# Kernel optimization log

Measured on AMD Instinct MI355X. Metric: run time of the kernel, lower is better.

The kernel has to match this reference:

```python
import jax, jax.numpy as jnp
import numpy as np

DIM = 2048            # model dim
HID = 4096            # ssm inner dim (multiple_of*round(2/3*6144))
H = 64                # n_heads
P = HID // H          # head_dim = 64
N = 128               # state_dim
G = 1                 # n_groups
K = 4                 # conv_size
Q = 128               # chunk_size
CONV_DIM = HID + 2 * G * N       # 4352
D_IN = 2 * HID + 2 * G * N + H   # 8512
EPS = 1e-5


def _causal_conv_silu(xBC, w):
    # xBC: [B,L,C], w: [C,K]; depthwise causal conv1d fused with SiLU
    kern = w.T[:, None, :]  # [K,1,C]
    y = jax.lax.conv_general_dilated(
        xBC, kern, window_strides=(1,), padding=[(K - 1, 0)],
        dimension_numbers=('NHC', 'HIO', 'NHC'),
        feature_group_count=xBC.shape[-1])
    return y * jax.nn.sigmoid(y)


def _ssm(x, W_in, conv_w, dt_bias, A_log, D, norm_w, W_out):
    Bsz, L, _ = x.shape
    zxbcdt = x @ W_in.T                       # [B,L,D_IN]
    z = zxbcdt[..., :HID]                     # gate
    xBC = zxbcdt[..., HID:HID + CONV_DIM]
    dt_raw = zxbcdt[..., HID + CONV_DIM:]     # [B,L,H]

    xBC = _causal_conv_silu(xBC, conv_w)
    xs = xBC[..., :HID].reshape(Bsz, L, H, P)
    rep = H // G
    Bh = jnp.repeat(xBC[..., HID:HID + G * N].reshape(Bsz, L, G, N), rep, axis=2)  # [B,L,H,N]
    Ch = jnp.repeat(xBC[..., HID + G * N:].reshape(Bsz, L, G, N), rep, axis=2)

    dt = jax.nn.softplus(dt_raw + dt_bias)    # [B,L,H], dt_softplus=True
    A = -jnp.exp(A_log)                       # [H]

    # ---- chunked selective scan (Mamba2 SSD), chunk size Q ----
    nc = L // Q
    a = (dt * A).reshape(Bsz, nc, Q, H)
    cum = jnp.cumsum(a, axis=2)               # inclusive within-chunk cumsum, <= 0
    xs_c = xs.reshape(Bsz, nc, Q, H, P)
    dtc = dt.reshape(Bsz, nc, Q, H)
    Bc = Bh.reshape(Bsz, nc, Q, H, N)
    Cc = Ch.reshape(Bsz, nc, Q, H, N)

    # intra-chunk (diagonal) part: Y[i] += sum_{j<=i} exp(cum_i-cum_j) dt_j (C_i.B_j) x_j
    diff = cum[:, :, :, None, :] - cum[:, :, None, :, :]     # [b,c,i,j,h]
    tril = jnp.tril(jnp.ones((Q, Q), bool))[None, None, :, :, None]
    Lmat = jnp.exp(jnp.where(tril, diff, -jnp.inf))          # causal decay matrix
    CB = jnp.einsum('bcihn,bcjhn->bcijh', Cc, Bc)
    M = CB * Lmat * dtc[:, :, None, :, :]
    Yd = jnp.einsum('bcijh,bcjhp->bcihp', M, xs_c)

    # per-chunk end state: sum_j exp(cum_last-cum_j) dt_j x_j (x) B_j
    wdec = jnp.exp(cum[:, :, -1:, :] - cum) * dtc            # [b,c,q,h]
    states = jnp.einsum('bcqh,bcqhn,bcqhp->bchpn', wdec, Bc, xs_c)
    chunk_decay = jnp.exp(cum[:, :, -1, :])                  # [b,c,h]

    # inter-chunk recurrence over nc chunks
    def step(S, inp):
        dec, st = inp                                        # [b,h], [b,h,p,n]
        return S * dec[..., None, None] + st, S              # emit state entering chunk
    S0 = jnp.zeros((Bsz, H, P, N), x.dtype)
    _, Sprev = jax.lax.scan(step, S0,
                            (chunk_decay.transpose(1, 0, 2),
                             states.transpose(1, 0, 2, 3, 4)))
    Sprev = Sprev.transpose(1, 0, 2, 3, 4)                   # [b,c,h,p,n]

    # inter-chunk (off-diagonal) contribution
    Yoff = jnp.einsum('bcqh,bcqhn,bchpn->bcqhp', jnp.exp(cum), Cc, Sprev)

    y = (Yd + Yoff).reshape(Bsz, L, H, P) + D[None, None, :, None] * xs  # skip D
    y = y.reshape(Bsz, L, HID)

    yz = y * (z * jax.nn.sigmoid(z))                         # gated: y * silu(z)
    yn = yz * jax.lax.rsqrt(jnp.mean(yz * yz, axis=-1, keepdims=True) + EPS) * norm_w
    return yn @ W_out.T


def setup_inputs() -> dict:
    key = jax.random.key(0)
    k = jax.random.split(key, 6)
    return {
        'x': jax.random.normal(k[0], (2, 4096, DIM), jnp.float32),
        'W_in': jax.random.normal(k[1], (D_IN, DIM), jnp.float32) * DIM ** -0.5,
        'conv_w': jax.random.normal(k[2], (CONV_DIM, K), jnp.float32) * K ** -0.5,
        'dt_bias': jax.random.uniform(k[3], (H,), jnp.float32, minval=0.001, maxval=0.1),
        'A_log': jnp.log(jax.random.uniform(k[4], (H,), jnp.float32, minval=1.0, maxval=16.0)),
        'D': jnp.ones((H,), jnp.float32),
        'norm_w': jnp.ones((HID,), jnp.float32),
        'W_out': jax.random.normal(k[5], (DIM, HID), jnp.float32) * HID ** -0.5,
    }


def reference(x, W_in, conv_w, dt_bias, A_log, D, norm_w, W_out):
    return _ssm(x, W_in, conv_w, dt_bias, A_log, D, norm_w, W_out)
```

## Files before the change

### kernel.cpp

```cpp
#include <hip/hip_runtime.h>
#include <hip/hip_fp16.h>
#include <math.h>

#define ROWS   8192
#define DIMK   2048
#define HIDN   4096
#define QCH    128
#define NCHUNK 32

typedef __attribute__((ext_vector_type(8))) short short8;
typedef __attribute__((ext_vector_type(8))) _Float16 half8;
typedef __attribute__((ext_vector_type(4))) float floatx4;

static __device__ inline unsigned short f2h(float f){
  union { _Float16 h; unsigned short u; } v; v.h = (_Float16)f; return v.u;
}
static __device__ inline float h2f(unsigned short u){
  union { unsigned short u; _Float16 h; } v; v.u = u; return (float)v.h;
}
static __device__ inline void async_cp16(const void* g, void* l){
  __builtin_amdgcn_global_load_lds((const __attribute__((address_space(1))) void*)g,
                                   (__attribute__((address_space(3))) void*)l, 16, 0, 0);
}

__global__ void k_cast(const float* __restrict__ in, unsigned short* __restrict__ out, int n4){
  int i = blockIdx.x * 256 + threadIdx.x;
  if (i < n4){
    float4 v = ((const float4*)in)[i];
    unsigned long long p = (unsigned long long)f2h(v.x)
                         | ((unsigned long long)f2h(v.y) << 16)
                         | ((unsigned long long)f2h(v.z) << 32)
                         | ((unsigned long long)f2h(v.w) << 48);
    ((unsigned long long*)out)[i] = p;
  }
}

#define DT_KT 128
__global__ __launch_bounds__(256)
void k_dtraw(const float* __restrict__ x, const float* __restrict__ Win,
             float* __restrict__ dtraw){
  __shared__ float ws[64 * (DT_KT + 4)];
  const int t = threadIdx.x;
  const int lane = t & 63, w = t >> 6;
  const int r0 = blockIdx.x * 8;
  const int rw = __builtin_amdgcn_readfirstlane(r0 + w * 2);
  float acc0 = 0.f, acc1 = 0.f;
  for (int k0 = 0; k0 < DIMK; k0 += DT_KT){
    __syncthreads();
#pragma unroll
    for (int l = 0; l < 8; l++){
      int fidx = (l * 256 + t) * 4;
      int row = fidx >> 7, col = fidx & 127;
      *(float4*)&ws[row * 132 + col] =
          *(const float4*)&Win[(size_t)(8448 + row) * DIMK + k0 + col];
    }
    __syncthreads();
    const float* xa = x + (size_t)rw * DIMK + k0;
    const float* xb = xa + DIMK;
#pragma unroll 8
    for (int kk = 0; kk < DT_KT; kk += 4){
      float4 wv = *(const float4*)&ws[lane * 132 + kk];
      float4 va = *(const float4*)&xa[kk];
      float4 vb = *(const float4*)&xb[kk];
      acc0 += wv.x*va.x + wv.y*va.y + wv.z*va.z + wv.w*va.w;
      acc1 += wv.x*vb.x + wv.y*vb.y + wv.z*vb.z + wv.w*vb.w;
    }
  }
  dtraw[(size_t)rw * 64 + lane]       = acc0;
  dtraw[(size_t)(rw + 1) * 64 + lane] = acc1;
}

__device__ inline void gemm_core(const unsigned short* __restrict__ A,
                                 const unsigned short* __restrict__ B,
                                 int Kd, int row0, int col0,
                                 unsigned short* lA, unsigned short* lB,
                                 floatx4 (&acc)[4][4], int t){
  const int w = t >> 6, lane = t & 63;
  const int quad = lane >> 4, l16 = lane & 15;
  const int wr = (w >> 1) * 64, wc = (w & 1) * 64;
  for (int k0 = 0; k0 < Kd; k0 += 64){
#pragma unroll
    for (int i = 0; i < 4; i++){
      int cb = i * 256 + w * 64, c = cb + lane;
      async_cp16(A + (size_t)(row0 + (c >> 3)) * Kd + k0 + (c & 7) * 8, lA + (size_t)cb * 8);
    }
#pragma unroll
    for (int i = 0; i < 4; i++){
      int cb = i * 256 + w * 64, c = cb + lane;
      async_cp16(B + (size_t)(col0 + (c >> 3)) * Kd + k0 + (c & 7) * 8, lB + (size_t)cb * 8);
    }
    __syncthreads();
#pragma unroll
    for (int ks = 0; ks < 2; ks++){
      half8 af[4], bfr[4];
#pragma unroll
      for (int i = 0; i < 4; i++){
        af[i]  = *(const half8*)&lA[(wr + i*16 + l16)*64 + ks*32 + quad*8];
        bfr[i] = *(const half8*)&lB[(wc + i*16 + l16)*64 + ks*32 + quad*8];
      }
#pragma unroll
      for (int i = 0; i < 4; i++)
#pragma unroll
        for (int j = 0; j < 4; j++)
          acc[i][j] = __builtin_amdgcn_mfma_f32_16x16x32_f16(af[i], bfr[j], acc[i][j], 0, 0, 0);
    }
    __syncthreads();
  }
}

__global__ __launch_bounds__(256, 2)
void k_gemm1(const unsigned short* __restrict__ A, const unsigned short* __restrict__ B,
             unsigned short* __restrict__ zbuf, unsigned short* __restrict__ xsraw,
             unsigned short* __restrict__ bcraw){
  __shared__ __align__(16) unsigned short lA[128*64];
  __shared__ __align__(16) unsigned short lB[128*64];
  const int t = threadIdx.x;
  const int row0 = blockIdx.y * 128, col0 = blockIdx.x * 128;
  floatx4 acc[4][4] = {};
  gemm_core(A, B, DIMK, row0, col0, lA, lB, acc, t);
  const int w = t >> 6, lane = t & 63, quad = lane >> 4, l16 = lane & 15;
  const int wr = (w >> 1) * 64, wc = (w & 1) * 64;
  unsigned short* dst; int cbase, ldd;
  if (col0 < 4096){ dst = zbuf; cbase = 0; ldd = 4096; }
  else if (col0 < 8192){ dst = xsraw; cbase = 4096; ldd = 4096; }
  else { dst = bcraw; cbase = 8192; ldd = 256; }
#pragma unroll
  for (int i = 0; i < 4; i++)
#pragma unroll
    for (int j = 0; j < 4; j++){
      int rb = row0 + wr + i*16 + quad*4;
      int cc = col0 + wc + j*16 + l16 - cbase;
#pragma unroll
      for (int r = 0; r < 4; r++)
        dst[(size_t)(rb + r) * ldd + cc] = f2h(acc[i][j][r]);
    }
}

__global__ __launch_bounds__(256, 2)
void k_gemm2(const unsigned short* __restrict__ A, const unsigned short* __restrict__ B,
             float* __restrict__ C){
  __shared__ __align__(16) unsigned short lA[128*64];
  __shared__ __align__(16) unsigned short lB[128*64];
  const int t = threadIdx.x;
  const int row0 = blockIdx.y * 128, col0 = blockIdx.x * 128;
  floatx4 acc[4][4] = {};
  gemm_core(A, B, HIDN, row0, col0, lA, lB, acc, t);
  const int w = t >> 6, lane = t & 63, quad = lane >> 4, l16 = lane & 15;
  const int wr = (w >> 1) * 64, wc = (w & 1) * 64;
#pragma unroll
  for (int i = 0; i < 4; i++)
#pragma unroll
    for (int j = 0; j < 4; j++){
      int rb = row0 + wr + i*16 + quad*4;
      int cc = col0 + wc + j*16 + l16;
#pragma unroll
      for (int r = 0; r < 4; r++)
        C[(size_t)(rb + r) * DIMK + cc] = acc[i][j][r];
    }
}

__global__ void k_halo(const unsigned short* __restrict__ xsraw, unsigned short* __restrict__ halo){
  int col = blockIdx.x * 256 + threadIdx.x;
  int slot = blockIdx.y, bc = blockIdx.z;
  long r = (long)bc * QCH - 3 + slot;
  if (r >= 0)
    halo[((size_t)bc * 3 + slot) * 4096 + col] = xsraw[(size_t)r * 4096 + col];
}

__global__ void k_convbc(const unsigned short* __restrict__ bcraw, const float* __restrict__ cw,
                         unsigned short* __restrict__ bcc){
  int row = blockIdx.x, c = threadIdx.x;
  int tl = row & 4095;
  const float4 wv = *(const float4*)&cw[(size_t)(4096 + c) * 4];
  const unsigned short* col = bcraw + c;
  size_t rb = (size_t)row * 256;
  float a = h2f(col[rb]) * wv.w;
  if (tl >= 1) a += h2f(col[rb - 256]) * wv.z;
  if (tl >= 2) a += h2f(col[rb - 512]) * wv.y;
  if (tl >= 3) a += h2f(col[rb - 768]) * wv.x;
  bcc[rb + c] = f2h(a / (1.f + __expf(-a)));
}

__global__ void k_dtcum(const float* __restrict__ dtraw, const float* __restrict__ dtbias,
                        const float* __restrict__ Alog, float* __restrict__ dtb,
                        float* __restrict__ cumb){
  int bc = blockIdx.x;
  int h  = threadIdx.x;
  float bias = dtbias[h];
  float A = -__expf(Alog[h]);
  float run = 0.f;
  size_t rowb = (size_t)bc * QCH;
  for (int q = 0; q < QCH; q++){
    float dr = dtraw[(rowb + q) * 64 + h] + bias;
    float dt = dr > 20.f ? dr : log1pf(__expf(dr));
    dtb[(rowb + q) * 64 + h] = dt;
    run += dt * A;
    cumb[(rowb + q) * 64 + h] = run;
  }
}

__device__ inline void stage_xsT(const unsigned short* __restrict__ xsraw,
                                 const unsigned short* __restrict__ halo,
                                 const float* cws, unsigned short* xsT,
                                 int bc, int h, int t){
  const size_t rowb = (size_t)bc * QCH;
  const int tl0 = (bc & 31) * QCH;
#pragma unroll
  for (int it = 0; it < 2; it++){
    int idx = it * 256 + t;
    int q = idx & 127, p0 = (idx >> 7) * 16;
    int tl = tl0 + q;
    const unsigned short* cur = xsraw + (rowb + q) * 4096 + h * 64 + p0;
    const unsigned short* hb  = halo + ((size_t)bc * 3) * 4096 + h * 64 + p0;
    const unsigned short* r1 = (q >= 1) ? cur - 4096     : hb + 2 * 4096;
    const unsigned short* r2 = (q >= 2) ? cur - 2 * 4096 : hb + (size_t)(q + 1) * 4096;
    const unsigned short* r3 = (q >= 3) ? cur - 3 * 4096 : hb + (size_t)q * 4096;
    float f1 = (tl >= 1) ? 1.f : 0.f;
    float f2 = (tl >= 2) ? 1.f : 0.f;
    float f3 = (tl >= 3) ? 1.f : 0.f;
    short8 c0 = *(const short8*)cur, c1 = *(const short8*)(cur + 8);
    short8 a0 = *(const short8*)r1,  a1 = *(const short8*)(r1 + 8);
    short8 b0 = *(const short8*)r2,  b1 = *(const short8*)(r2 + 8);
    short8 d0 = *(const short8*)r3,  d1 = *(const short8*)(r3 + 8);
#pragma unroll
    for (int j = 0; j < 16; j++){
      int col = p0 + j;
      const float* wp = cws + col * 4;
      float vc = h2f((unsigned short)(j < 8 ? c0[j] : c1[j-8]));
      float v1 = h2f((unsigned short)(j < 8 ? a0[j] : a1[j-8]));
      float v2 = h2f((unsigned short)(j < 8 ? b0[j] : b1[j-8]));
      float v3 = h2f((unsigned short)(j < 8 ? d0[j] : d1[j-8]));
      float a = vc * wp[3] + f1 * v1 * wp[2] + f2 * v2 * wp[1] + f3 * v3 * wp[0];
      float s = a / (1.f + __expf(-a));
      xsT[col * 128 + q] = f2h(s);
    }
  }
}

__global__ __launch_bounds__(256, 2)
void k_chunk1(const unsigned short* __restrict__ xsraw, const unsigned short* __restrict__ bcc,
              const unsigned short* __restrict__ halo, const float* __restrict__ cw,
              const float* __restrict__ dtb, const float* __restrict__ cumb,
              const float* __restrict__ Dp, const unsigned short* __restrict__ st,
              unsigned short* __restrict__ ybuf){
  __shared__ __align__(16) unsigned short Ml[128*128];
  __shared__ __align__(16) unsigned short xsT[64*128];
  __shared__ float cum_s[128], dt_s[128];
  __shared__ float cws[64*4];
  const int blk = blockIdx.x, h = blk & 63, bc = blk >> 6;
  const size_t rowb = (size_t)bc * QCH;
  const int t = threadIdx.x, w = t >> 6, lane = t & 63, quad = lane >> 4, l16 = lane & 15;
  const int wrow = w * 32;
  if (t < 128){ cum_s[t] = cumb[(rowb + t)*64 + h]; dt_s[t] = dtb[(rowb + t)*64 + h]; }
  if (t < 64) *(float4*)&cws[t*4] = *(const float4*)&cw[((size_t)h*64 + t)*4];
  __syncthreads();
  stage_xsT(xsraw, halo, cws, xsT, bc, h, t);
  floatx4 acc[2][8] = {};
  const unsigned short* Cb = bcc + rowb * 256 + 128;
  const unsigned short* Bb = bcc + rowb * 256;
#pragma unroll
  for (int ks = 0; ks < 4; ks++){
    half8 af[2];
#pragma unroll
    for (int i = 0; i < 2; i++)
      af[i] = *(const half8*)(Cb + (size_t)(wrow + i*16 + l16) * 256 + ks*32 + quad*8);
#pragma unroll
    for (int j = 0; j < 8; j++){
      half8 bfr = *(const half8*)(Bb + (size_t)(j*16 + l16) * 256 + ks*32 + quad*8);
#pragma unroll
      for (int i = 0; i < 2; i++)
        acc[i][j] = __builtin_amdgcn_mfma_f32_16x16x32_f16(af[i], bfr, acc[i][j], 0, 0, 0);
    }
  }
#pragma unroll
  for (int i = 0; i < 2; i++)
#pragma unroll
    for (int j = 0; j < 8; j++){
      int jc = j*16 + l16;
      float dtj = dt_s[jc], cj = cum_s[jc];
#pragma unroll
      for (int r = 0; r < 4; r++){
        int ir = wrow + i*16 + quad*4 + r;
        float m = (ir >= jc) ? acc[i][j][r] * __expf(cum_s[ir] - cj) * dtj : 0.f;
        Ml[ir * 128 + jc] = f2h(m);
      }
    }
  __syncthreads();
  floatx4 accY[2][4] = {};
#pragma unroll
  for (int ks = 0; ks < 4; ks++){
    half8 af[2], bfr[4];
#pragma unroll
    for (int i = 0; i < 2; i++)
      af[i] = *(const half8*)&Ml[(wrow + i*16 + l16)*128 + ks*32 + quad*8];
#pragma unroll
    for (int p = 0; p < 4; p++)
      bfr[p] = *(const half8*)&xsT[(p*16 + l16)*128 + ks*32 + quad*8];
#pragma unroll
    for (int i = 0; i < 2; i++)
#pragma unroll
      for (int p = 0; p < 4; p++)
        accY[i][p] = __builtin_amdgcn_mfma_f32_16x16x32_f16(af[i], bfr[p], accY[i][p], 0, 0, 0);
  }
  __syncthreads();
  unsigned short* Sp = Ml;
  {
    size_t base = ((size_t)bc * 64 + h) * 8192;
#pragma unroll
    for (int it = 0; it < 4; it++){
      int idx = (it * 256 + t) * 8;
      *(short8*)&Sp[idx] = *(const short8*)&st[base + idx];
    }
  }
  __syncthreads();
  floatx4 accO[2][4] = {};
#pragma unroll
  for (int ks = 0; ks < 4; ks++){
    half8 af[2], bfr[4];
#pragma unroll
    for (int i = 0; i < 2; i++)
      af[i] = *(const half8*)(Cb + (size_t)(wrow + i*16 + l16) * 256 + ks*32 + quad*8);
#pragma unroll
    for (int p = 0; p < 4; p++)
      bfr[p] = *(const half8*)&Sp[(p*16 + l16)*128 + ks*32 + quad*8];
#pragma unroll
    for (int i = 0; i < 2; i++)
#pragma unroll
      for (int p = 0; p < 4; p++)
        accO[i][p] = __builtin_amdgcn_mfma_f32_16x16x32_f16(af[i], bfr[p], accO[i][p], 0, 0, 0);
  }
  float Dh = Dp[h];
#pragma unroll
  for (int i = 0; i < 2; i++)
#pragma unroll
    for (int p = 0; p < 4; p++){
      int pc = p*16 + l16;
#pragma unroll
      for (int r = 0; r < 4; r++){
        int ir = wrow + i*16 + quad*4 + r;
        float y = accY[i][p][r] + __expf(cum_s[ir]) * accO[i][p][r] + Dh * h2f(xsT[pc*128 + ir]);
        ybuf[(rowb + ir) * (size_t)HIDN + h*64 + pc] = f2h(y);
      }
    }
}

__global__ __launch_bounds__(256, 2)
void k_chunk2(const unsigned short* __restrict__ xsraw, const unsigned short* __restrict__ bcc,
              const unsigned short* __restrict__ halo, const float* __restrict__ cw,
              const float* __restrict__ dtb, const float* __restrict__ cumb,
              unsigned short* __restrict__ st){
  __shared__ __align__(16) unsigned short wBT[128*128];
  __shared__ __align__(16) unsigned short xsT[64*128];
  __shared__ float cum_s[128], dt_s[128];
  __shared__ float cws[64*4];
  const int blk = blockIdx.x, h = blk & 63, bc = blk >> 6;
  const size_t rowb = (size_t)bc * QCH;
  const int t = threadIdx.x, w = t >> 6, lane = t & 63, quad = lane >> 4, l16 = lane & 15;
  if (t < 128){ cum_s[t] = cumb[(rowb + t)*64 + h]; dt_s[t] = dtb[(rowb + t)*64 + h]; }
  if (t < 64) *(float4*)&cws[t*4] = *(const float4*)&cw[((size_t)h*64 + t)*4];
  __syncthreads();
  stage_xsT(xsraw, halo, cws, xsT, bc, h, t);
  float clast = cum_s[127];
#pragma unroll
  for (int it = 0; it < 2; it++){
    int idx = it * 256 + t;
    int q = idx & 127, n0 = (idx >> 7) * 32;
    float wd = __expf(clast - cum_s[q]) * dt_s[q];
    const unsigned short* gp = bcc + (rowb + q) * 256 + n0;
#pragma unroll
    for (int c4 = 0; c4 < 4; c4++){
      short8 v = *(const short8*)(gp + c4*8);
#pragma unroll
      for (int jj = 0; jj < 8; jj++)
        wBT[(n0 + c4*8 + jj)*128 + q] = f2h(h2f((unsigned short)v[jj]) * wd);
    }
  }
  __syncthreads();
  floatx4 acc[8] = {};
#pragma unroll
  for (int ks = 0; ks < 4; ks++){
    half8 af = *(const half8*)&xsT[(w*16 + l16)*128 + ks*32 + quad*8];
#pragma unroll
    for (int j = 0; j < 8; j++){
      half8 bfr = *(const half8*)&wBT[(j*16 + l16)*128 + ks*32 + quad*8];
      acc[j] = __builtin_amdgcn_mfma_f32_16x16x32_f16(af, bfr, acc[j], 0, 0, 0);
    }
  }
  size_t base = ((size_t)bc * 64 + h) * 8192;
#pragma unroll
  for (int j = 0; j < 8; j++){
    int n = j*16 + l16;
#pragma unroll
    for (int r = 0; r < 4; r++){
      int p = w*16 + quad*4 + r;
      st[base + p*128 + n] = f2h(acc[j][r]);
    }
  }
}

__global__ void k_scan(unsigned short* __restrict__ st, const float* __restrict__ cumb){
  int id = blockIdx.x * 256 + threadIdx.x;
  int n = id & 127, p = (id >> 7) & 63, h = (id >> 13) & 63, b = id >> 19;
  float S = 0.f;
  for (int c = 0; c < NCHUNK; c++){
    int bc = b * NCHUNK + c;
    size_t idx = ((size_t)bc * 64 + h) * 8192 + (size_t)p * 128 + n;
    float dec = __expf(cumb[((size_t)bc * QCH + 127) * 64 + h]);
    float v = h2f(st[idx]);
    st[idx] = f2h(S);
    S = S * dec + v;
  }
}

__global__ __launch_bounds__(256)
void k_gate(unsigned short* __restrict__ yb, const unsigned short* __restrict__ zb,
            const float* __restrict__ nw){
  __shared__ float red[4];
  int row = blockIdx.x, t = threadIdx.x;
  float vals[16], ss = 0.f;
#pragma unroll
  for (int it = 0; it < 16; it++){
    int c = it * 256 + t;
    float y = h2f(yb[(size_t)row * HIDN + c]);
    float z = h2f(zb[(size_t)row * HIDN + c]);
    float v = y * (z / (1.f + __expf(-z)));
    vals[it] = v; ss += v * v;
  }
  for (int o = 32; o > 0; o >>= 1) ss += __shfl_down(ss, o, 64);
  int w = t >> 6, lane = t & 63;
  if (lane == 0) red[w] = ss;
  __syncthreads();
  float scale = rsqrtf((red[0] + red[1] + red[2] + red[3]) / (float)HIDN + 1e-5f);
#pragma unroll
  for (int it = 0; it < 16; it++){
    int c = it * 256 + t;
    yb[(size_t)row * HIDN + c] = f2h(vals[it] * scale * nw[c]);
  }
}

extern "C" void kernel_launch(void* const* d_in, const int* in_sizes, int n_in,
                              void* d_out, int out_size, void* d_ws, size_t ws_size,
                              hipStream_t stream){
  const float* x      = (const float*)d_in[0];
  const float* Win    = (const float*)d_in[1];
  const float* convw  = (const float*)d_in[2];
  const float* dtbias = (const float*)d_in[3];
  const float* Alog   = (const float*)d_in[4];
  const float* Dp     = (const float*)d_in[5];
  const float* nw     = (const float*)d_in[6];
  const float* Wout   = (const float*)d_in[7];
  float* out = (float*)d_out;

  char* ws = (char*)d_ws;
  size_t off = 0;
  auto alloc = [&](size_t bytes)->void*{ void* p = ws + off; off += (bytes + 255) & ~(size_t)255; return p; };
  unsigned short* xw    = (unsigned short*)alloc((size_t)ROWS * DIMK * 2);
  unsigned short* winb  = (unsigned short*)alloc((size_t)8448 * DIMK * 2);
  float*          dtraw = (float*)alloc((size_t)ROWS * 64 * 4);
  unsigned short* woutb = (unsigned short*)alloc((size_t)DIMK * HIDN * 2);
  unsigned short* zbuf  = (unsigned short*)alloc((size_t)ROWS * HIDN * 2);
  unsigned short* xsraw = (unsigned short*)alloc((size_t)ROWS * HIDN * 2);
  unsigned short* bcraw = (unsigned short*)alloc((size_t)ROWS * 256 * 2);
  unsigned short* bcc   = (unsigned short*)alloc((size_t)ROWS * 256 * 2);
  unsigned short* halo  = (unsigned short*)alloc((size_t)64 * 3 * 4096 * 2);
  float*          dtb   = (float*)alloc((size_t)ROWS * 64 * 4);
  float*          cumb  = (float*)alloc((size_t)ROWS * 64 * 4);
  unsigned short* st    = xw;
  unsigned short* ybuf  = xsraw;

  k_cast<<<(ROWS*DIMK/4 + 255)/256, 256, 0, stream>>>(x, xw, ROWS*DIMK/4);
  k_cast<<<(8448*DIMK/4 + 255)/256, 256, 0, stream>>>(Win, winb, 8448*DIMK/4);
  k_cast<<<(DIMK*HIDN/4 + 255)/256, 256, 0, stream>>>(Wout, woutb, DIMK*HIDN/4);
  k_dtraw<<<ROWS/8, 256, 0, stream>>>(x, Win, dtraw);
  k_gemm1<<<dim3(66, ROWS/128), 256, 0, stream>>>(xw, winb, zbuf, xsraw, bcraw);
  k_halo<<<dim3(16, 3, 64), 256, 0, stream>>>(xsraw, halo);
  k_convbc<<<ROWS, 256, 0, stream>>>(bcraw, convw, bcc);
  k_dtcum<<<64, 64, 0, stream>>>(dtraw, dtbias, Alog, dtb, cumb);
  k_chunk2<<<4096, 256, 0, stream>>>(xsraw, bcc, halo, convw, dtb, cumb, st);
  k_scan<<<4096, 256, 0, stream>>>(st, cumb);
  k_chunk1<<<4096, 256, 0, stream>>>(xsraw, bcc, halo, convw, dtb, cumb, Dp, st, ybuf);
  k_gate<<<ROWS, 256, 0, stream>>>(ybuf, zbuf, nw);
  k_gemm2<<<dim3(16, ROWS/128), 256, 0, stream>>>(ybuf, woutb, out);
}
```

Before: 1.186 ms.

## Use 256x256 double-buffered swizzled-LDS GEMM tiles with 512 threads

Replaces the 128x128 single-buffered GEMM core with a 256x256 tile computed by 8 waves, double-buffered async global-to-LDS loads, an XOR swizzle on the LDS layout to avoid bank conflicts, and s_setprio around the MFMA blocks. Block indices are remapped so neighbouring blocks share tiles, which should improve L2 reuse. The aim is more arithmetic per loaded byte and overlap of loads with MFMA work in both projection GEMMs. In exchange it uses 128KB of LDS per block and many more accumulator registers, and gemm2 launches only 256 blocks, which may not fill the GPU.

```diff
diff --git a/kernel.cpp b/kernel.cpp
--- a/kernel.cpp
+++ b/kernel.cpp
@@ -70,92 +70,137 @@
   dtraw[(size_t)(rw + 1) * 64 + lane] = acc1;
 }
 
-__device__ inline void gemm_core(const unsigned short* __restrict__ A,
-                                 const unsigned short* __restrict__ B,
-                                 int Kd, int row0, int col0,
-                                 unsigned short* lA, unsigned short* lB,
-                                 floatx4 (&acc)[4][4], int t){
-  const int w = t >> 6, lane = t & 63;
+template<int KD>
+__device__ inline void gemm256_core(const unsigned short* __restrict__ A,
+                                    const unsigned short* __restrict__ B,
+                                    int row0, int col0,
+                                    unsigned short* sA, unsigned short* sB,
+                                    floatx4 (&acc)[8][4], int t){
+  const int lane = t & 63, wid = t >> 6;
+  const int wm = wid >> 2, wn = wid & 3;
   const int quad = lane >> 4, l16 = lane & 15;
-  const int wr = (w >> 1) * 64, wc = (w & 1) * 64;
-  for (int k0 = 0; k0 < Kd; k0 += 64){
-#pragma unroll
-    for (int i = 0; i < 4; i++){
-      int cb = i * 256 + w * 64, c = cb + lane;
-      async_cp16(A + (size_t)(row0 + (c >> 3)) * Kd + k0 + (c & 7) * 8, lA + (size_t)cb * 8);
-    }
-#pragma unroll
-    for (int i = 0; i < 4; i++){
-      int cb = i * 256 + w * 64, c = cb + lane;
-      async_cp16(B + (size_t)(col0 + (c >> 3)) * Kd + k0 + (c & 7) * 8, lB + (size_t)cb * 8);
-    }
-    __syncthreads();
-#pragma unroll
-    for (int ks = 0; ks < 2; ks++){
-      half8 af[4], bfr[4];
-#pragma unroll
-      for (int i = 0; i < 4; i++){
-        af[i]  = *(const half8*)&lA[(wr + i*16 + l16)*64 + ks*32 + quad*8];
-        bfr[i] = *(const half8*)&lB[(wc + i*16 + l16)*64 + ks*32 + quad*8];
+  const int srow  = t >> 3;
+  const int sslot = (t & 7) ^ (srow & 7);
+  constexpr int NT = KD / 64;
+  unsigned short* bA[2] = { sA, sA + 256*64 };
+  unsigned short* bB[2] = { sB, sB + 256*64 };
+
+  auto stage = [&](unsigned short* dA, unsigned short* dB, int kt){
+    const int k0 = kt * 64;
+#pragma unroll
+    for (int i = 0; i < 4; i++)
+      async_cp16(A + (size_t)(row0 + i*64 + srow) * KD + k0 + sslot*8,
+                 dA + ((size_t)i*512 + t)*8);
+#pragma unroll
+    for (int i = 0; i < 4; i++)
+      async_cp16(B + (size_t)(col0 + i*64 + srow) * KD + k0 + sslot*8,
+                 dB + ((size_t)i*512 + t)*8);
+  };
+
+  stage(bA[0], bB[0], 0);
+  stage(bA[1], bB[1], 1);
+  asm volatile("s_waitcnt vmcnt(8)" ::: "memory");
+  __builtin_amdgcn_s_barrier();
+
+  int cur = 0;
+  for (int kt = 0; kt < NT; kt++){
+    const unsigned short* cA = bA[cur] + (size_t)wm * 128 * 64;
+    const unsigned short* cB = bB[cur] + (size_t)wn * 64 * 64;
+#pragma unroll
+    for (int mg = 0; mg < 2; mg++)
+#pragma unroll
+    for (int ng = 0; ng < 2; ng++){
+      half8 af[4][2], bf[2][2];
+#pragma unroll
+      for (int mm = 0; mm < 4; mm++){
+        int row = (mg*4 + mm)*16 + l16;
+#pragma unroll
+        for (int ks = 0; ks < 2; ks++)
+          af[mm][ks] = *(const half8*)&cA[row*64 + (((ks*4 + quad) ^ (l16 & 7)) * 8)];
       }
 #pragma unroll
-      for (int i = 0; i < 4; i++)
-#pragma unroll
-        for (int j = 0; j < 4; j++)
-          acc[i][j] = __builtin_amdgcn_mfma_f32_16x16x32_f16(af[i], bfr[j], acc[i][j], 0, 0, 0);
-    }
-    __syncthreads();
-  }
-}
-
-__global__ __launch_bounds__(256, 2)
+      for (int nn = 0; nn < 2; nn++){
+        int row = (ng*2 + nn)*16 + l16;
+#pragma unroll
+        for (int ks = 0; ks < 2; ks++)
+          bf[nn][ks] = *(const half8*)&cB[row*64 + (((ks*4 + quad) ^ (l16 & 7)) * 8)];
+      }
+      __builtin_amdgcn_s_setprio(1);
+#pragma unroll
+      for (int mm = 0; mm < 4; mm++)
+#pragma unroll
+      for (int nn = 0; nn < 2; nn++)
+#pragma unroll
+      for (int ks = 0; ks < 2; ks++)
+        acc[mg*4+mm][ng*2+nn] = __builtin_amdgcn_mfma_f32_16x16x32_f16(
+            af[mm][ks], bf[nn][ks], acc[mg*4+mm][ng*2+nn], 0, 0, 0);
+      __builtin_amdgcn_s_setprio(0);
+    }
+    if (kt == NT - 1) break;
+    __builtin_amdgcn_s_barrier();
+    if (kt + 2 < NT){
+      stage(bA[cur], bB[cur], kt + 2);
+      asm volatile("s_waitcnt vmcnt(8)" ::: "memory");
+    } else {
+      asm volatile("s_waitcnt vmcnt(0)" ::: "memory");
+    }
+    __builtin_amdgcn_s_barrier();
+    cur ^= 1;
+  }
+}
+
+__global__ __launch_bounds__(512, 2)
 void k_gemm1(const unsigned short* __restrict__ A, const unsigned short* __restrict__ B,
              unsigned short* __restrict__ zbuf, unsigned short* __restrict__ xsraw,
              unsigned short* __restrict__ bcraw){
-  __shared__ __align__(16) unsigned short lA[128*64];
-  __shared__ __align__(16) unsigned short lB[128*64];
+  __shared__ __align__(16) unsigned short sA[2*256*64];
+  __shared__ __align__(16) unsigned short sB[2*256*64];
   const int t = threadIdx.x;
-  const int row0 = blockIdx.y * 128, col0 = blockIdx.x * 128;
-  floatx4 acc[4][4] = {};
-  gemm_core(A, B, DIMK, row0, col0, lA, lB, acc, t);
-  const int w = t >> 6, lane = t & 63, quad = lane >> 4, l16 = lane & 15;
-  const int wr = (w >> 1) * 64, wc = (w & 1) * 64;
+  int swz = (blockIdx.x % 8) * 132 + blockIdx.x / 8;
+  const int row0 = (swz & 31) * 256, col0 = (swz >> 5) * 256;
+  floatx4 acc[8][4] = {};
+  gemm256_core<DIMK>(A, B, row0, col0, sA, sB, acc, t);
+  const int lane = t & 63, wid = t >> 6;
+  const int wm = wid >> 2, wn = wid & 3;
+  const int quad = lane >> 4, l16 = lane & 15;
   unsigned short* dst; int cbase, ldd;
   if (col0 < 4096){ dst = zbuf; cbase = 0; ldd = 4096; }
   else if (col0 < 8192){ dst = xsraw; cbase = 4096; ldd = 4096; }
   else { dst = bcraw; cbase = 8192; ldd = 256; }
 #pragma unroll
-  for (int i = 0; i < 4; i++)
-#pragma unroll
-    for (int j = 0; j < 4; j++){
-      int rb = row0 + wr + i*16 + quad*4;
-      int cc = col0 + wc + j*16 + l16 - cbase;
+  for (int m = 0; m < 8; m++)
+#pragma unroll
+    for (int n = 0; n < 4; n++){
+      int rb = row0 + wm*128 + m*16 + quad*4;
+      int cc = col0 + wn*64 + n*16 + l16 - cbase;
 #pragma unroll
       for (int r = 0; r < 4; r++)
-        dst[(size_t)(rb + r) * ldd + cc] = f2h(acc[i][j][r]);
-    }
-}
-
-__global__ __launch_bounds__(256, 2)
+        dst[(size_t)(rb + r) * ldd + cc] = f2h(acc[m][n][r]);
+    }
+}
+
+__global__ __launch_bounds__(512, 2)
 void k_gemm2(const unsigned short* __restrict__ A, const unsigned short* __restrict__ B,
              float* __restrict__ C){
-  __shared__ __align__(16) unsigned short lA[128*64];
-  __shared__ __align__(16) unsigned short lB[128*64];
+  __shared__ __align__(16) unsigned short sA[2*256*64];
+  __shared__ __align__(16) unsigned short sB[2*256*64];
   const int t = threadIdx.x;
-  const int row0 = blockIdx.y * 128, col0 = blockIdx.x * 128;
-  floatx4 acc[4][4] = {};
-  gemm_core(A, B, HIDN, row0, col0, lA, lB, acc, t);
-  const int w = t >> 6, lane = t & 63, quad = lane >> 4, l16 = lane & 15;
-  const int wr = (w >> 1) * 64, wc = (w & 1) * 64;
-#pragma unroll
-  for (int i = 0; i < 4; i++)
-#pragma unroll
-    for (int j = 0; j < 4; j++){
-      int rb = row0 + wr + i*16 + quad*4;
-      int cc = col0 + wc + j*16 + l16;
+  int swz = (blockIdx.x % 8) * 32 + blockIdx.x / 8;
+  const int row0 = (swz & 31) * 256, col0 = (swz >> 5) * 256;
+  floatx4 acc[8][4] = {};
+  gemm256_core<HIDN>(A, B, row0, col0, sA, sB, acc, t);
+  const int lane = t & 63, wid = t >> 6;
+  const int wm = wid >> 2, wn = wid & 3;
+  const int quad = lane >> 4, l16 = lane & 15;
+#pragma unroll
+  for (int m = 0; m < 8; m++)
+#pragma unroll
+    for (int n = 0; n < 4; n++){
+      int rb = row0 + wm*128 + m*16 + quad*4;
+      int cc = col0 + wn*64 + n*16 + l16;
 #pragma unroll
       for (int r = 0; r < 4; r++)
-        C[(size_t)(rb + r) * DIMK + cc] = acc[i][j][r];
+        C[(size_t)(rb + r) * DIMK + cc] = acc[m][n][r];
     }
 }
 
@@ -472,7 +517,7 @@
   k_cast<<<(8448*DIMK/4 + 255)/256, 256, 0, stream>>>(Win, winb, 8448*DIMK/4);
   k_cast<<<(DIMK*HIDN/4 + 255)/256, 256, 0, stream>>>(Wout, woutb, DIMK*HIDN/4);
   k_dtraw<<<ROWS/8, 256, 0, stream>>>(x, Win, dtraw);
-  k_gemm1<<<dim3(66, ROWS/128), 256, 0, stream>>>(xw, winb, zbuf, xsraw, bcraw);
+  k_gemm1<<<dim3(33*32), 512, 0, stream>>>(xw, winb, zbuf, xsraw, bcraw);
   k_halo<<<dim3(16, 3, 64), 256, 0, stream>>>(xsraw, halo);
   k_convbc<<<ROWS, 256, 0, stream>>>(bcraw, convw, bcc);
   k_dtcum<<<64, 64, 0, stream>>>(dtraw, dtbias, Alog, dtb, cumb);
@@ -480,5 +525,5 @@
   k_scan<<<4096, 256, 0, stream>>>(st, cumb);
   k_chunk1<<<4096, 256, 0, stream>>>(xsraw, bcc, halo, convw, dtb, cumb, Dp, st, ybuf);
   k_gate<<<ROWS, 256, 0, stream>>>(ybuf, zbuf, nw);
-  k_gemm2<<<dim3(16, ROWS/128), 256, 0, stream>>>(ybuf, woutb, out);
-}
+  k_gemm2<<<dim3(8*32), 512, 0, stream>>>(ybuf, woutb, out);
+}
```

Result: slower. 1.570 ms (+32.4%).
